# Optimization experiments

Hardware: AMD Instinct MI355X
Metric: run time of the kernel (lower is better)

The kernel has to match this reference:

```python
import jax, jax.numpy as jnp
import numpy as np

NUM_HEADS = 32
NUM_KV_HEADS = 8
HEAD_DIM = 128
EPS = 1e-5
ROPE_THETA = 10000.0


def _rope(x, positions):
    # x: [S, H, D] (NeoX-style rotate-half), positions: [S] int
    half = HEAD_DIM // 2
    inv_freq = 1.0 / (ROPE_THETA ** (jnp.arange(0, HEAD_DIM, 2, dtype=jnp.float32) / HEAD_DIM))
    freqs = positions.astype(jnp.float32)[:, None] * inv_freq  # [S, half]
    cos = jnp.concatenate([jnp.cos(freqs), jnp.cos(freqs)], axis=-1)[:, None, :]  # [S,1,D]
    sin = jnp.concatenate([jnp.sin(freqs), jnp.sin(freqs)], axis=-1)[:, None, :]
    x1, x2 = x[..., :half], x[..., half:]
    rot = jnp.concatenate([-x2, x1], axis=-1)
    return x * cos + rot * sin


def setup_inputs() -> dict:
    key = jax.random.key(0)
    k1, k2, k3 = jax.random.split(key, 3)
    S, H = 2048, 4096
    q_size = NUM_HEADS * HEAD_DIM
    kv_size = NUM_KV_HEADS * HEAD_DIM
    return {
        "positions": jnp.arange(S, dtype=jnp.int32),
        "hidden_states": jax.random.normal(k1, (S, H), dtype=jnp.float32),
        "layernorm_weight": jnp.ones((H,), dtype=jnp.float32),
        "w_qkv": jax.random.normal(k2, (q_size + 2 * kv_size, H), dtype=jnp.float32) * (H ** -0.5),
        "w_o": jax.random.normal(k3, (H, q_size), dtype=jnp.float32) * (q_size ** -0.5),
    }


def reference(positions, hidden_states, layernorm_weight, w_qkv, w_o):
    S, H = hidden_states.shape
    # Fused RMSNorm (computed in f32) + QKV projection
    x32 = hidden_states.astype(jnp.float32)
    var = jnp.mean(x32 * x32, axis=-1, keepdims=True)
    xn = x32 * jax.lax.rsqrt(var + EPS) * layernorm_weight
    qkv = xn @ w_qkv.T  # [S, (Hq+2*Hkv)*D]
    q_size = NUM_HEADS * HEAD_DIM
    kv_size = NUM_KV_HEADS * HEAD_DIM
    q = qkv[:, :q_size].reshape(S, NUM_HEADS, HEAD_DIM)
    k = qkv[:, q_size:q_size + kv_size].reshape(S, NUM_KV_HEADS, HEAD_DIM)
    v = qkv[:, q_size + kv_size:].reshape(S, NUM_KV_HEADS, HEAD_DIM)
    # RoPE on q, k
    q = _rope(q, positions)
    k = _rope(k, positions)
    # GQA: expand kv heads to query heads
    group = NUM_HEADS // NUM_KV_HEADS
    k = jnp.repeat(k, group, axis=1)  # [S, Hq, D]
    v = jnp.repeat(v, group, axis=1)
    scale = HEAD_DIM ** -0.5
    scores = jnp.einsum('qhd,khd->hqk', q, k) * scale  # [Hq, S, S]
    mask = positions[:, None] >= positions[None, :]  # causal
    scores = jnp.where(mask[None, :, :], scores, jnp.finfo(scores.dtype).min)
    probs = jax.nn.softmax(scores, axis=-1)
    attn = jnp.einsum('hqk,khd->qhd', probs, v).reshape(S, q_size)
    out = attn @ w_o.T  # [S, H]
    return out.astype(hidden_states.dtype)
```

## Files before the change

kernel.cpp:

```cpp
#include <hip/hip_runtime.h>
#include <stdint.h>
#include <type_traits>


typedef __bf16 bf16x8 __attribute__((ext_vector_type(8)));
typedef float f32x4 __attribute__((ext_vector_type(4)));

#define S_LEN 2048
#define HDIM 4096
#define QKV_N 6144
#define NQH 32
#define NKVH 8
#define HD 128

__device__ __forceinline__ float bf2f(uint16_t u){
    union { uint32_t u; float f; } v; v.u = ((uint32_t)u) << 16; return v.f;
}
__device__ __forceinline__ uint16_t f2bf(float f){
    union { float f; uint32_t u; } v; v.f = f;
    uint32_t u = v.u;
    return (uint16_t)((u + 0x7FFFu + ((u >> 16) & 1u)) >> 16);
}

__device__ __forceinline__ void gload_lds16(uint16_t* lds_dst, const uint16_t* g_src){
    __builtin_amdgcn_global_load_lds(
        (const __attribute__((address_space(1))) void*)(g_src),
        (__attribute__((address_space(3))) void*)(lds_dst),
        16, 0, 0);
}

__global__ __launch_bounds__(256) void prep_k(const float* __restrict__ w_qkv,
                                              const float* __restrict__ w_o,
                                              const float* __restrict__ x,
                                              const float* __restrict__ lw,
                                              uint16_t* __restrict__ wqkv_b,
                                              uint16_t* __restrict__ wo_b,
                                              uint16_t* __restrict__ xn){
    int b = blockIdx.x;
    int t = threadIdx.x;
    if (b < 20480){
        const float* src; uint16_t* dst; size_t i;
        if (b < 12288){ src = w_qkv; dst = wqkv_b; i = (size_t)b * 2048 + t * 8; }
        else          { src = w_o;   dst = wo_b;   i = (size_t)(b - 12288) * 2048 + t * 8; }
        float4 a = *(const float4*)(src + i);
        float4 c = *(const float4*)(src + i + 4);
        uint16_t o[8];
        o[0] = f2bf(a.x); o[1] = f2bf(a.y); o[2] = f2bf(a.z); o[3] = f2bf(a.w);
        o[4] = f2bf(c.x); o[5] = f2bf(c.y); o[6] = f2bf(c.z); o[7] = f2bf(c.w);
        *(uint4*)(dst + i) = *(uint4*)o;
        return;
    }
    int row = b - 20480;
    const float* xr = x + (size_t)row * HDIM + t * 16;
    float f[16];
#pragma unroll
    for (int p = 0; p < 4; ++p) *(float4*)(f + p * 4) = *(const float4*)(xr + p * 4);
    float ss = 0.f;
#pragma unroll
    for (int i = 0; i < 16; ++i) ss += f[i] * f[i];
#pragma unroll
    for (int off = 32; off > 0; off >>= 1) ss += __shfl_down(ss, off);
    __shared__ float red[4];
    if ((t & 63) == 0) red[t >> 6] = ss;
    __syncthreads();
    float tot = red[0] + red[1] + red[2] + red[3];
    float inv = rsqrtf(tot * (1.0f / HDIM) + 1e-5f);
    float wf[16];
#pragma unroll
    for (int p = 0; p < 4; ++p) *(float4*)(wf + p * 4) = *(const float4*)(lw + t * 16 + p * 4);
    uint16_t o[16];
#pragma unroll
    for (int i = 0; i < 16; ++i) o[i] = f2bf(f[i] * inv * wf[i]);
    uint16_t* outp = xn + (size_t)row * HDIM + t * 16;
    *(uint4*)(outp)     = *(uint4*)(o);
    *(uint4*)(outp + 8) = *(uint4*)(o + 8);
}

template <typename OutT>
__global__ __launch_bounds__(256, 2) void gemm_bt_k(const uint16_t* __restrict__ A,
                                                    const uint16_t* __restrict__ B,
                                                    OutT* __restrict__ C,
                                                    int M, int N, int K){
    __shared__ uint16_t lA[128 * 64];
    __shared__ uint16_t lB[128 * 64];
    int t = threadIdx.x;
    int lane = t & 63;
    int w = t >> 6;
    int wm = w >> 1, wn = w & 1;
    int quad = lane >> 4, ln = lane & 15;
    int tileM = blockIdx.y * 128, tileN = blockIdx.x * 128;

    f32x4 acc[4][4];
#pragma unroll
    for (int i = 0; i < 4; ++i)
#pragma unroll
      for (int j = 0; j < 4; ++j) acc[i][j] = (f32x4){0.f, 0.f, 0.f, 0.f};

    for (int k0 = 0; k0 < K; k0 += 64){
        __syncthreads();
#pragma unroll
        for (int it = 0; it < 4; ++it){
            int pp = it * 256 + t;
            int row = pp >> 3, cc = pp & 7;
            int gcc = cc ^ (row & 7);
            gload_lds16(&lA[pp * 8], A + (size_t)(tileM + row) * K + k0 + gcc * 8);
            gload_lds16(&lB[pp * 8], B + (size_t)(tileN + row) * K + k0 + gcc * 8);
        }
        __syncthreads();
#pragma unroll
        for (int kk = 0; kk < 64; kk += 32){
            int cc = (kk + quad * 8) >> 3;
            bf16x8 aF[4], bF[4];
#pragma unroll
            for (int i = 0; i < 4; ++i){
                int ra = wm * 64 + i * 16 + ln;
                aF[i] = *(const bf16x8*)&lA[ra * 64 + ((cc ^ (ra & 7)) * 8)];
                int rb = wn * 64 + i * 16 + ln;
                bF[i] = *(const bf16x8*)&lB[rb * 64 + ((cc ^ (rb & 7)) * 8)];
            }
#pragma unroll
            for (int i = 0; i < 4; ++i)
#pragma unroll
                for (int j = 0; j < 4; ++j)
                    acc[i][j] = __builtin_amdgcn_mfma_f32_16x16x32_bf16(aF[i], bF[j], acc[i][j], 0, 0, 0);
        }
    }
#pragma unroll
    for (int i = 0; i < 4; ++i)
#pragma unroll
      for (int r = 0; r < 4; ++r){
          int row = tileM + wm * 64 + i * 16 + quad * 4 + r;
#pragma unroll
          for (int j = 0; j < 4; ++j){
              int col = tileN + wn * 64 + j * 16 + ln;
              if constexpr (std::is_same<OutT, float>::value)
                  C[(size_t)row * N + col] = acc[i][j][r];
              else
                  C[(size_t)row * N + col] = f2bf(acc[i][j][r]);
          }
      }
}

__global__ __launch_bounds__(256) void ropevt_k(const int* __restrict__ pos,
                                                uint16_t* __restrict__ qkv,
                                                uint16_t* __restrict__ vT){
    int b = blockIdx.x;
    int t = threadIdx.x;
    if (b < 2048){
        int s = b;
        float fpos = (float)pos[s];
        uint16_t* rowp = qkv + (size_t)s * QKV_N;
#pragma unroll
        for (int rep = 0; rep < 3; ++rep){
            int g = t + rep * 256;
            if (rep == 2 && t >= 128) break;
            int head = g >> 4;
            int i4 = (g & 15) * 4;
            int col = (head < NQH) ? head * HD : HDIM + (head - NQH) * HD;
            uint16_t* p1 = rowp + col + i4;
            uint16_t* p2 = p1 + 64;
            ushort4 u1 = *(ushort4*)p1;
            ushort4 u2 = *(ushort4*)p2;
            uint16_t e1[4] = {u1.x, u1.y, u1.z, u1.w};
            uint16_t e2[4] = {u2.x, u2.y, u2.z, u2.w};
            uint16_t o1[4], o2[4];
#pragma unroll
            for (int e = 0; e < 4; ++e){
                float j = (float)(i4 + e);
                float inv = __expf(j * -0.14391156831212787f);
                float fr = fpos * inv;
                float sn, c;
                __sincosf(fr, &sn, &c);
                float x1 = bf2f(e1[e]), x2 = bf2f(e2[e]);
                o1[e] = f2bf(x1 * c - x2 * sn);
                o2[e] = f2bf(x2 * c + x1 * sn);
            }
            *(ushort4*)p1 = make_ushort4(o1[0], o1[1], o1[2], o1[3]);
            *(ushort4*)p2 = make_ushort4(o2[0], o2[1], o2[2], o2[3]);
        }
        return;
    }
    __shared__ uint16_t tile[64][65];
    int bx = b - 2048;
    int ts = (bx & 31) * 64;
    int tc = (bx >> 5) * 64;
#pragma unroll
    for (int p = 0; p < 16; ++p){
        int lin = p * 256 + t;
        int r = lin >> 6, c = lin & 63;
        tile[r][c] = qkv[(size_t)(ts + r) * QKV_N + (HDIM + 1024) + tc + c];
    }
    __syncthreads();
#pragma unroll
    for (int p = 0; p < 16; ++p){
        int lin = p * 256 + t;
        int r = lin >> 6, c = lin & 63;
        vT[(size_t)(tc + r) * S_LEN + ts + c] = tile[c][r];
    }
}

__global__ __launch_bounds__(256, 2) void attn_k(const uint16_t* __restrict__ qkv,
                                                 const uint16_t* __restrict__ vT,
                                                 uint16_t* __restrict__ attn){
    __shared__ uint16_t lK[2][64 * 128];
    __shared__ uint16_t lV[2][64 * 128];
    __shared__ uint16_t lP[4 * 2048];
    int bid = blockIdx.x;
    int h = bid & 31;
    int z = bid >> 5;
    int qt = (z < 8) ? 15 - z : z - 8;
    int kvh = h >> 2;
    int t = threadIdx.x, lane = t & 63, w = t >> 6;
    int quad = lane >> 4, ln = lane & 15;
    int qBase = qt * 128 + w * 32;

    const float scale = 0.1275174316788196f;

    bf16x8 qF[2][4];
#pragma unroll
    for (int i = 0; i < 2; ++i)
#pragma unroll
      for (int kk = 0; kk < 4; ++kk){
          int row = qBase + i * 16 + ln;
          bf16x8 raw = *(const bf16x8*)(qkv + (size_t)row * QKV_N + h * HD + kk * 32 + quad * 8);
#pragma unroll
          for (int e = 0; e < 8; ++e){
              union { __bf16 b; uint16_t u; } cv; cv.b = raw[e];
              union { uint16_t u; __bf16 b; } cw; cw.u = f2bf(bf2f(cv.u) * scale);
              raw[e] = cw.b;
          }
          qF[i][kk] = raw;
      }

    f32x4 oAcc[2][8];
#pragma unroll
    for (int i = 0; i < 2; ++i)
#pragma unroll
      for (int j = 0; j < 8; ++j) oAcc[i][j] = (f32x4){0.f, 0.f, 0.f, 0.f};
    float lsum[2][4];
#pragma unroll
    for (int i = 0; i < 2; ++i)
#pragma unroll
      for (int r = 0; r < 4; ++r) lsum[i][r] = 0.f;

    uint16_t* pB = lP + w * 2048;

    int nkt = 2 * qt + 2;

    #define STAGE(KT, B)                                                            \
    {                                                                               \
        _Pragma("unroll")                                                           \
        for (int it = 0; it < 4; ++it){                                             \
            int pp = it * 256 + t;                                                  \
            int row = pp >> 4, cc = pp & 15;                                        \
            int gcc = cc ^ (row & 7);                                               \
            gload_lds16(&lK[B][pp * 8],                                             \
                        qkv + (size_t)((KT) * 64 + row) * QKV_N + HDIM + kvh * HD + gcc * 8); \
            int rowv = pp >> 3, ccv = pp & 7;                                       \
            int gccv = ccv ^ (rowv & 7);                                            \
            gload_lds16(&lV[B][pp * 8],                                             \
                        vT + (size_t)(kvh * HD + rowv) * S_LEN + (KT) * 64 + gccv * 8); \
        }                                                                           \
    }

    STAGE(0, 0);
    __syncthreads();

    for (int kt = 0; kt < nkt; ++kt){
        int cur = kt & 1;
        if (kt + 1 < nkt) STAGE(kt + 1, cur ^ 1);

        f32x4 sAcc[2][4];
#pragma unroll
        for (int i = 0; i < 2; ++i)
#pragma unroll
          for (int j = 0; j < 4; ++j) sAcc[i][j] = (f32x4){0.f, 0.f, 0.f, 0.f};

        __builtin_amdgcn_s_setprio(1);
#pragma unroll
        for (int kk = 0; kk < 4; ++kk){
            int cc = kk * 4 + quad;
            bf16x8 bF[4];
#pragma unroll
            for (int j = 0; j < 4; ++j){
                int row = j * 16 + ln;
                bF[j] = *(const bf16x8*)&lK[cur][row * 128 + ((cc ^ (row & 7)) * 8)];
            }
#pragma unroll
            for (int i = 0; i < 2; ++i)
#pragma unroll
              for (int j = 0; j < 4; ++j)
                  sAcc[i][j] = __builtin_amdgcn_mfma_f32_16x16x32_bf16(qF[i][kk], bF[j], sAcc[i][j], 0, 0, 0);
        }
        __builtin_amdgcn_s_setprio(0);

        bool diag = (kt >= nkt - 2);
#pragma unroll
        for (int i = 0; i < 2; ++i)
#pragma unroll
          for (int r = 0; r < 4; ++r){
              int qrow = qBase + i * 16 + quad * 4 + r;
              int prow = i * 16 + quad * 4 + r;
              int pbase = prow * 64 + (ln & 7);
              int bsel = ln >> 3, ssel = prow & 7;
              float part = 0.f;
#pragma unroll
              for (int j = 0; j < 4; ++j){
                  float sv = sAcc[i][j][r];
                  if (diag){
                      int colg = kt * 64 + j * 16 + ln;
                      if (colg > qrow) sv = -1e30f;
                  }
                  float pv = exp2f(sv);
                  part += pv;
                  pB[pbase + (((2 * j + bsel) ^ ssel) * 8)] = f2bf(pv);
              }
              lsum[i][r] += part;
          }

        __builtin_amdgcn_s_setprio(1);
#pragma unroll
        for (int kk = 0; kk < 2; ++kk){
            int cc = kk * 4 + quad;
            bf16x8 aP[2];
#pragma unroll
            for (int i = 0; i < 2; ++i){
                int row = i * 16 + ln;
                aP[i] = *(const bf16x8*)&pB[row * 64 + (((cc ^ (row & 7)) & 7) * 8)];
            }
            bf16x8 bV[8];
#pragma unroll
            for (int j = 0; j < 8; ++j){
                int row = j * 16 + ln;
                bV[j] = *(const bf16x8*)&lV[cur][row * 64 + (((cc ^ (row & 7)) & 7) * 8)];
            }
#pragma unroll
            for (int i = 0; i < 2; ++i)
#pragma unroll
              for (int j = 0; j < 8; ++j)
                  oAcc[i][j] = __builtin_amdgcn_mfma_f32_16x16x32_bf16(aP[i], bV[j], oAcc[i][j], 0, 0, 0);
        }
        __builtin_amdgcn_s_setprio(0);

        __syncthreads();
    }
    #undef STAGE

#pragma unroll
    for (int i = 0; i < 2; ++i)
#pragma unroll
      for (int r = 0; r < 4; ++r){
          float l = lsum[i][r];
#pragma unroll
          for (int off = 1; off < 16; off <<= 1) l += __shfl_xor(l, off);
          float invl = 1.0f / l;
          int row = qBase + i * 16 + quad * 4 + r;
#pragma unroll
          for (int j = 0; j < 8; ++j)
              attn[(size_t)row * HDIM + h * HD + j * 16 + ln] = f2bf(oAcc[i][j][r] * invl);
      }
}

extern "C" void kernel_launch(void* const* d_in, const int* in_sizes, int n_in,
                              void* d_out, int out_size, void* d_ws, size_t ws_size,
                              hipStream_t stream){
    const int*   positions = (const int*)d_in[0];
    const float* hidden    = (const float*)d_in[1];
    const float* lw        = (const float*)d_in[2];
    const float* w_qkv     = (const float*)d_in[3];
    const float* w_o       = (const float*)d_in[4];
    float* out = (float*)d_out;

    uint16_t* xn     = (uint16_t*)d_ws;
    uint16_t* qkv    = xn     + (size_t)S_LEN * HDIM;
    uint16_t* vT     = qkv    + (size_t)S_LEN * QKV_N;
    uint16_t* attn   = vT     + (size_t)NKVH * HD * S_LEN;
    uint16_t* wqkv_b = attn   + (size_t)S_LEN * HDIM;
    uint16_t* wo_b   = wqkv_b + (size_t)QKV_N * HDIM;

    prep_k<<<22528, 256, 0, stream>>>(w_qkv, w_o, hidden, lw, wqkv_b, wo_b, xn);
    gemm_bt_k<uint16_t><<<dim3(QKV_N / 128, S_LEN / 128), 256, 0, stream>>>(xn, wqkv_b, qkv, S_LEN, QKV_N, HDIM);
    ropevt_k<<<2560, 256, 0, stream>>>(positions, qkv, vT);
    attn_k<<<NQH * (S_LEN / 128), 256, 0, stream>>>(qkv, vT, attn);
    gemm_bt_k<float><<<dim3(HDIM / 128, S_LEN / 128), 256, 0, stream>>>(attn, wo_b, out, S_LEN, HDIM, HDIM);
}
```

Measured before the change: 485.6 us.

## Fuse RoPE into QKV GEMM epilogue and skip fully masked attention tiles

Moves the RoPE rotation into the QKV GEMM epilogue. The B-column mapping is remapped so each wave holds both rotate-half partners (col and col+64) in registers, which removes a separate read-modify-write pass over q and k. The standalone rope kernel becomes a V-transpose-only kernel. The attention kernel now skips the QK/softmax/PV work for key tiles lying entirely above the causal diagonal for a warp's rows, and uses the native bf16 conversion instead of manual rounding. The risks are a different rounding path and extra transcendentals in the GEMM epilogue.

```diff
diff --git a/kernel.cpp b/kernel.cpp
--- a/kernel.cpp
+++ b/kernel.cpp
@@ -20,6 +20,9 @@
     union { float f; uint32_t u; } v; v.f = f;
     uint32_t u = v.u;
     return (uint16_t)((u + 0x7FFFu + ((u >> 16) & 1u)) >> 16);
+}
+__device__ __forceinline__ uint16_t f2bf_n(float f){
+    union { __bf16 b; uint16_t u; } v; v.b = (__bf16)f; return v.u;
 }
 
 __device__ __forceinline__ void gload_lds16(uint16_t* lds_dst, const uint16_t* g_src){
@@ -76,11 +79,12 @@
     *(uint4*)(outp + 8) = *(uint4*)(o + 8);
 }
 
-template <typename OutT>
+template <typename OutT, bool ROPE>
 __global__ __launch_bounds__(256, 2) void gemm_bt_k(const uint16_t* __restrict__ A,
                                                     const uint16_t* __restrict__ B,
                                                     OutT* __restrict__ C,
-                                                    int M, int N, int K){
+                                                    int M, int N, int K,
+                                                    const int* __restrict__ pos){
     __shared__ uint16_t lA[128 * 64];
     __shared__ uint16_t lB[128 * 64];
     int t = threadIdx.x;
@@ -115,7 +119,7 @@
             for (int i = 0; i < 4; ++i){
                 int ra = wm * 64 + i * 16 + ln;
                 aF[i] = *(const bf16x8*)&lA[ra * 64 + ((cc ^ (ra & 7)) * 8)];
-                int rb = wn * 64 + i * 16 + ln;
+                int rb = wn * 32 + (i & 1) * 16 + (i >> 1) * 64 + ln;
                 bF[i] = *(const bf16x8*)&lB[rb * 64 + ((cc ^ (rb & 7)) * 8)];
             }
 #pragma unroll
@@ -125,6 +129,30 @@
                     acc[i][j] = __builtin_amdgcn_mfma_f32_16x16x32_bf16(aF[i], bF[j], acc[i][j], 0, 0, 0);
         }
     }
+    if constexpr (ROPE){
+        if (tileN < 5120){
+            const float c0 = -0.20762050593046014f;
+            float invf0 = exp2f((float)(wn * 32 + ln) * c0);
+            float invf1 = exp2f((float)(wn * 32 + 16 + ln) * c0);
+#pragma unroll
+            for (int i = 0; i < 4; ++i)
+#pragma unroll
+              for (int r = 0; r < 4; ++r){
+                  int row = tileM + wm * 64 + i * 16 + quad * 4 + r;
+                  float fp = (float)pos[row];
+#pragma unroll
+                  for (int jp = 0; jp < 2; ++jp){
+                      float sn, cs;
+                      __sincosf(fp * (jp ? invf1 : invf0), &sn, &cs);
+                      float x1 = acc[i][jp][r], x2 = acc[i][jp + 2][r];
+                      int c1 = tileN + wn * 32 + jp * 16 + ln;
+                      C[(size_t)row * N + c1]      = f2bf(x1 * cs - x2 * sn);
+                      C[(size_t)row * N + c1 + 64] = f2bf(x2 * cs + x1 * sn);
+                  }
+              }
+            return;
+        }
+    }
 #pragma unroll
     for (int i = 0; i < 4; ++i)
 #pragma unroll
@@ -132,7 +160,7 @@
           int row = tileM + wm * 64 + i * 16 + quad * 4 + r;
 #pragma unroll
           for (int j = 0; j < 4; ++j){
-              int col = tileN + wn * 64 + j * 16 + ln;
+              int col = tileN + wn * 32 + (j & 1) * 16 + (j >> 1) * 64 + ln;
               if constexpr (std::is_same<OutT, float>::value)
                   C[(size_t)row * N + col] = acc[i][j][r];
               else
@@ -141,47 +169,11 @@
       }
 }
 
-__global__ __launch_bounds__(256) void ropevt_k(const int* __restrict__ pos,
-                                                uint16_t* __restrict__ qkv,
+__global__ __launch_bounds__(256) void vtrans_k(const uint16_t* __restrict__ qkv,
                                                 uint16_t* __restrict__ vT){
-    int b = blockIdx.x;
+    __shared__ uint16_t tile[64][65];
+    int bx = blockIdx.x;
     int t = threadIdx.x;
-    if (b < 2048){
-        int s = b;
-        float fpos = (float)pos[s];
-        uint16_t* rowp = qkv + (size_t)s * QKV_N;
-#pragma unroll
-        for (int rep = 0; rep < 3; ++rep){
-            int g = t + rep * 256;
-            if (rep == 2 && t >= 128) break;
-            int head = g >> 4;
-            int i4 = (g & 15) * 4;
-            int col = (head < NQH) ? head * HD : HDIM + (head - NQH) * HD;
-            uint16_t* p1 = rowp + col + i4;
-            uint16_t* p2 = p1 + 64;
-            ushort4 u1 = *(ushort4*)p1;
-            ushort4 u2 = *(ushort4*)p2;
-            uint16_t e1[4] = {u1.x, u1.y, u1.z, u1.w};
-            uint16_t e2[4] = {u2.x, u2.y, u2.z, u2.w};
-            uint16_t o1[4], o2[4];
-#pragma unroll
-            for (int e = 0; e < 4; ++e){
-                float j = (float)(i4 + e);
-                float inv = __expf(j * -0.14391156831212787f);
-                float fr = fpos * inv;
-                float sn, c;
-                __sincosf(fr, &sn, &c);
-                float x1 = bf2f(e1[e]), x2 = bf2f(e2[e]);
-                o1[e] = f2bf(x1 * c - x2 * sn);
-                o2[e] = f2bf(x2 * c + x1 * sn);
-            }
-            *(ushort4*)p1 = make_ushort4(o1[0], o1[1], o1[2], o1[3]);
-            *(ushort4*)p2 = make_ushort4(o2[0], o2[1], o2[2], o2[3]);
-        }
-        return;
-    }
-    __shared__ uint16_t tile[64][65];
-    int bx = b - 2048;
     int ts = (bx & 31) * 64;
     int tc = (bx >> 5) * 64;
 #pragma unroll
@@ -270,77 +262,79 @@
         int cur = kt & 1;
         if (kt + 1 < nkt) STAGE(kt + 1, cur ^ 1);
 
-        f32x4 sAcc[2][4];
-#pragma unroll
-        for (int i = 0; i < 2; ++i)
-#pragma unroll
-          for (int j = 0; j < 4; ++j) sAcc[i][j] = (f32x4){0.f, 0.f, 0.f, 0.f};
-
-        __builtin_amdgcn_s_setprio(1);
-#pragma unroll
-        for (int kk = 0; kk < 4; ++kk){
-            int cc = kk * 4 + quad;
-            bf16x8 bF[4];
-#pragma unroll
-            for (int j = 0; j < 4; ++j){
-                int row = j * 16 + ln;
-                bF[j] = *(const bf16x8*)&lK[cur][row * 128 + ((cc ^ (row & 7)) * 8)];
+        if (kt * 64 <= qBase + 31){
+            f32x4 sAcc[2][4];
+#pragma unroll
+            for (int i = 0; i < 2; ++i)
+#pragma unroll
+              for (int j = 0; j < 4; ++j) sAcc[i][j] = (f32x4){0.f, 0.f, 0.f, 0.f};
+
+            __builtin_amdgcn_s_setprio(1);
+#pragma unroll
+            for (int kk = 0; kk < 4; ++kk){
+                int cc = kk * 4 + quad;
+                bf16x8 bF[4];
+#pragma unroll
+                for (int j = 0; j < 4; ++j){
+                    int row = j * 16 + ln;
+                    bF[j] = *(const bf16x8*)&lK[cur][row * 128 + ((cc ^ (row & 7)) * 8)];
+                }
+#pragma unroll
+                for (int i = 0; i < 2; ++i)
+#pragma unroll
+                  for (int j = 0; j < 4; ++j)
+                      sAcc[i][j] = __builtin_amdgcn_mfma_f32_16x16x32_bf16(qF[i][kk], bF[j], sAcc[i][j], 0, 0, 0);
             }
+            __builtin_amdgcn_s_setprio(0);
+
+            bool diag = (kt >= nkt - 2);
 #pragma unroll
             for (int i = 0; i < 2; ++i)
 #pragma unroll
-              for (int j = 0; j < 4; ++j)
-                  sAcc[i][j] = __builtin_amdgcn_mfma_f32_16x16x32_bf16(qF[i][kk], bF[j], sAcc[i][j], 0, 0, 0);
+              for (int r = 0; r < 4; ++r){
+                  int qrow = qBase + i * 16 + quad * 4 + r;
+                  int prow = i * 16 + quad * 4 + r;
+                  int pbase = prow * 64 + (ln & 7);
+                  int bsel = ln >> 3, ssel = prow & 7;
+                  float part = 0.f;
+#pragma unroll
+                  for (int j = 0; j < 4; ++j){
+                      float sv = sAcc[i][j][r];
+                      if (diag){
+                          int colg = kt * 64 + j * 16 + ln;
+                          if (colg > qrow) sv = -1e30f;
+                      }
+                      float pv = exp2f(sv);
+                      part += pv;
+                      pB[pbase + (((2 * j + bsel) ^ ssel) * 8)] = f2bf_n(pv);
+                  }
+                  lsum[i][r] += part;
+              }
+
+            __builtin_amdgcn_s_setprio(1);
+#pragma unroll
+            for (int kk = 0; kk < 2; ++kk){
+                int cc = kk * 4 + quad;
+                bf16x8 aP[2];
+#pragma unroll
+                for (int i = 0; i < 2; ++i){
+                    int row = i * 16 + ln;
+                    aP[i] = *(const bf16x8*)&pB[row * 64 + (((cc ^ (row & 7)) & 7) * 8)];
+                }
+                bf16x8 bV[8];
+#pragma unroll
+                for (int j = 0; j < 8; ++j){
+                    int row = j * 16 + ln;
+                    bV[j] = *(const bf16x8*)&lV[cur][row * 64 + (((cc ^ (row & 7)) & 7) * 8)];
+                }
+#pragma unroll
+                for (int i = 0; i < 2; ++i)
+#pragma unroll
+                  for (int j = 0; j < 8; ++j)
+                      oAcc[i][j] = __builtin_amdgcn_mfma_f32_16x16x32_bf16(aP[i], bV[j], oAcc[i][j], 0, 0, 0);
+            }
+            __builtin_amdgcn_s_setprio(0);
         }
-        __builtin_amdgcn_s_setprio(0);
-
-        bool diag = (kt >= nkt - 2);
-#pragma unroll
-        for (int i = 0; i < 2; ++i)
-#pragma unroll
-          for (int r = 0; r < 4; ++r){
-              int qrow = qBase + i * 16 + quad * 4 + r;
-              int prow = i * 16 + quad * 4 + r;
-              int pbase = prow * 64 + (ln & 7);
-              int bsel = ln >> 3, ssel = prow & 7;
-              float part = 0.f;
-#pragma unroll
-              for (int j = 0; j < 4; ++j){
-                  float sv = sAcc[i][j][r];
-                  if (diag){
-                      int colg = kt * 64 + j * 16 + ln;
-                      if (colg > qrow) sv = -1e30f;
-                  }
-                  float pv = exp2f(sv);
-                  part += pv;
-                  pB[pbase + (((2 * j + bsel) ^ ssel) * 8)] = f2bf(pv);
-              }
-              lsum[i][r] += part;
-          }
-
-        __builtin_amdgcn_s_setprio(1);
-#pragma unroll
-        for (int kk = 0; kk < 2; ++kk){
-            int cc = kk * 4 + quad;
-            bf16x8 aP[2];
-#pragma unroll
-            for (int i = 0; i < 2; ++i){
-                int row = i * 16 + ln;
-                aP[i] = *(const bf16x8*)&pB[row * 64 + (((cc ^ (row & 7)) & 7) * 8)];
-            }
-            bf16x8 bV[8];
-#pragma unroll
-            for (int j = 0; j < 8; ++j){
-                int row = j * 16 + ln;
-                bV[j] = *(const bf16x8*)&lV[cur][row * 64 + (((cc ^ (row & 7)) & 7) * 8)];
-            }
-#pragma unroll
-            for (int i = 0; i < 2; ++i)
-#pragma unroll
-              for (int j = 0; j < 8; ++j)
-                  oAcc[i][j] = __builtin_amdgcn_mfma_f32_16x16x32_bf16(aP[i], bV[j], oAcc[i][j], 0, 0, 0);
-        }
-        __builtin_amdgcn_s_setprio(0);
 
         __syncthreads();
     }
@@ -357,7 +351,7 @@
           int row = qBase + i * 16 + quad * 4 + r;
 #pragma unroll
           for (int j = 0; j < 8; ++j)
-              attn[(size_t)row * HDIM + h * HD + j * 16 + ln] = f2bf(oAcc[i][j][r] * invl);
+              attn[(size_t)row * HDIM + h * HD + j * 16 + ln] = f2bf_n(oAcc[i][j][r] * invl);
       }
 }
 
@@ -379,8 +373,8 @@
     uint16_t* wo_b   = wqkv_b + (size_t)QKV_N * HDIM;
 
     prep_k<<<22528, 256, 0, stream>>>(w_qkv, w_o, hidden, lw, wqkv_b, wo_b, xn);
-    gemm_bt_k<uint16_t><<<dim3(QKV_N / 128, S_LEN / 128), 256, 0, stream>>>(xn, wqkv_b, qkv, S_LEN, QKV_N, HDIM);
-    ropevt_k<<<2560, 256, 0, stream>>>(positions, qkv, vT);
+    gemm_bt_k<uint16_t, true><<<dim3(QKV_N / 128, S_LEN / 128), 256, 0, stream>>>(xn, wqkv_b, qkv, S_LEN, QKV_N, HDIM, positions);
+    vtrans_k<<<512, 256, 0, stream>>>(qkv, vT);
     attn_k<<<NQH * (S_LEN / 128), 256, 0, stream>>>(qkv, vT, attn);
-    gemm_bt_k<float><<<dim3(HDIM / 128, S_LEN / 128), 256, 0, stream>>>(attn, wo_b, out, S_LEN, HDIM, HDIM);
-}
+    gemm_bt_k<float, false><<<dim3(HDIM / 128, S_LEN / 128), 256, 0, stream>>>(attn, wo_b, out, S_LEN, HDIM, HDIM, positions);
+}
```

New measurement: 480.5 us. No clear change (-1.1%).
